# Performance work log

Measured on AMD Instinct MI355X. Metric: run time of the kernel, lower is better.

Reference implementation:

```python
import jax, jax.numpy as jnp
import numpy as np

B, D_MODEL, L = 4, 1024, 2048
D_STATE, D_CONV, EXPAND = 16, 4, 2
D_INNER = EXPAND * D_MODEL
DT_RANK = (D_MODEL + 15) // 16  # 64


def setup_inputs() -> dict:
    key = jax.random.key(0)
    ks = jax.random.split(key, 12)
    s = 0.02
    x = jax.random.normal(ks[0], (B, D_MODEL, L), dtype=jnp.float32)
    in_proj_w = jax.random.normal(ks[1], (2 * D_INNER, D_MODEL), dtype=jnp.float32) * s
    conv_w = jax.random.normal(ks[2], (D_INNER, D_CONV), dtype=jnp.float32) * 0.2
    conv_b = jnp.zeros((D_INNER,), dtype=jnp.float32)
    x_proj_w = jax.random.normal(ks[3], (DT_RANK + 2 * D_STATE, D_INNER), dtype=jnp.float32) * s
    dt_proj_w = jax.random.normal(ks[4], (D_INNER, DT_RANK), dtype=jnp.float32) * (DT_RANK ** -0.5)
    # bias init so softplus(bias) ~ dt in [1e-3, 1e-1], as in mamba_ssm
    dt = jnp.exp(jax.random.uniform(ks[5], (D_INNER,), dtype=jnp.float32)
                 * (np.log(0.1) - np.log(1e-3)) + np.log(1e-3))
    dt_proj_b = dt + jnp.log(-jnp.expm1(-dt))  # inverse softplus
    A_log = jnp.log(jnp.broadcast_to(jnp.arange(1, D_STATE + 1, dtype=jnp.float32),
                                     (D_INNER, D_STATE)))
    D = jnp.ones((D_INNER,), dtype=jnp.float32)
    out_proj_w = jax.random.normal(ks[6], (D_MODEL, D_INNER), dtype=jnp.float32) * s
    proj_w = jax.random.normal(ks[7], (D_MODEL, D_MODEL), dtype=jnp.float32) * s
    proj_b = jnp.zeros((D_MODEL,), dtype=jnp.float32)
    return dict(x=x, in_proj_w=in_proj_w, conv_w=conv_w, conv_b=conv_b,
                x_proj_w=x_proj_w, dt_proj_w=dt_proj_w, dt_proj_b=dt_proj_b,
                A_log=A_log, D=D, out_proj_w=out_proj_w, proj_w=proj_w, proj_b=proj_b)


def _mamba_forward(x, in_proj_w, conv_w, conv_b, x_proj_w, dt_proj_w, dt_proj_b,
                   A_log, D, out_proj_w, proj_w, proj_b):
    xt = jnp.transpose(x, (0, 2, 1))                      # (B, L, d_model)
    xz = jnp.einsum('bld,ed->ble', xt, in_proj_w)         # (B, L, 2*d_inner)
    u, z = jnp.split(xz, 2, axis=-1)                      # each (B, L, d_inner)

    # depthwise causal conv1d along time
    uc = jnp.transpose(u, (0, 2, 1))                      # (B, d_inner, L)
    upad = jnp.pad(uc, ((0, 0), (0, 0), (D_CONV - 1, 0)))
    conv = sum(conv_w[None, :, k, None] * upad[:, :, k:k + L] for k in range(D_CONV))
    conv = conv + conv_b[None, :, None]
    u = jax.nn.silu(jnp.transpose(conv, (0, 2, 1)))       # (B, L, d_inner)

    x_dbl = jnp.einsum('bld,ed->ble', u, x_proj_w)        # (B, L, dt_rank+2n)
    dt_low, Bm, Cm = jnp.split(x_dbl, [DT_RANK, DT_RANK + D_STATE], axis=-1)
    delta = jax.nn.softplus(jnp.einsum('blr,dr->bld', dt_low, dt_proj_w) + dt_proj_b)
    A = -jnp.exp(A_log)                                   # (d_inner, d_state)

    def step(h, inp):
        d_t, B_t, C_t, u_t = inp                          # (B,d),(B,n),(B,n),(B,d)
        dA = jnp.exp(d_t[:, :, None] * A[None])           # (B, d, n)
        dBu = d_t[:, :, None] * B_t[:, None, :] * u_t[:, :, None]
        h = dA * h + dBu
        y_t = jnp.einsum('bdn,bn->bd', h, C_t)
        return h, y_t

    xs = (jnp.transpose(delta, (1, 0, 2)), jnp.transpose(Bm, (1, 0, 2)),
          jnp.transpose(Cm, (1, 0, 2)), jnp.transpose(u, (1, 0, 2)))
    h0 = jnp.zeros((B, D_INNER, D_STATE), dtype=x.dtype)
    _, ys = jax.lax.scan(step, h0, xs)                    # ys: (L, B, d_inner)
    y = jnp.transpose(ys, (1, 0, 2)) + u * D              # (B, L, d_inner)
    y = y * jax.nn.silu(z)

    out = jnp.einsum('bld,ed->ble', y, out_proj_w)        # (B, L, d_model)
    out = jnp.einsum('bld,ed->ble', out, proj_w) + proj_b
    return jnp.transpose(out, (0, 2, 1))                  # (B, d_model, L)


def reference(x, in_proj_w, conv_w, conv_b, x_proj_w, dt_proj_w, dt_proj_b,
              A_log, D, out_proj_w, proj_w, proj_b):
    return _mamba_forward(x, in_proj_w, conv_w, conv_b, x_proj_w, dt_proj_w,
                          dt_proj_b, A_log, D, out_proj_w, proj_w, proj_b)
```

## Files before the change

kernel.cpp:

```cpp
#include <hip/hip_runtime.h>
#include <hip/hip_bf16.h>
#include <math.h>

#define BB 4
#define DMODEL 1024
#define LL 2048
#define DSTATE 16
#define DCONV 4
#define DINNER 2048
#define DTRANK 64
#define BL (BB * LL)
#define NCHUNK 32
#define LCH (LL / NCHUNK)
#define PFPLANE (BB * DINNER * DSTATE)
#define XPN 96
#define XPSPLIT 4
#define XPK (DINNER / XPSPLIT)

typedef unsigned short ushort;
typedef __bf16 bf16x8 __attribute__((ext_vector_type(8)));
typedef float f32x4 __attribute__((ext_vector_type(4)));

__device__ inline ushort f2bf(float f) {
    unsigned int u = __float_as_uint(f);
    u += 0x7fffu + ((u >> 16) & 1u);
    return (ushort)(u >> 16);
}
__device__ inline float bf2f(ushort h) {
    return __uint_as_float(((unsigned int)h) << 16);
}
__device__ inline float softplus_fast(float v) {
    float e = __expf(-fabsf(v));
    return fmaxf(v, 0.f) + __logf(1.f + e);
}

__device__ __forceinline__ void gload16(const ushort* g, ushort* l) {
    __builtin_amdgcn_global_load_lds(
        (__attribute__((address_space(1))) void*)g,
        (__attribute__((address_space(3))) void*)l, 16, 0, 0);
}

__global__ void f32_to_bf16(const float* __restrict__ src, ushort* __restrict__ dst, int n4) {
    int i = blockIdx.x * 256 + threadIdx.x;
    if (i < n4) {
        float4 v = ((const float4*)src)[i];
        ushort4 o;
        o.x = f2bf(v.x); o.y = f2bf(v.y); o.z = f2bf(v.z); o.w = f2bf(v.w);
        ((ushort4*)dst)[i] = o;
    }
}

__global__ void transpose_convert_x(const float* __restrict__ x, ushort* __restrict__ xtb) {
    __shared__ float tile[32][33];
    int b = blockIdx.z;
    int l0 = blockIdx.x * 32;
    int d0 = blockIdx.y * 32;
    int tx = threadIdx.x, ty = threadIdx.y;
    const float* xb = x + (size_t)b * DMODEL * LL;
#pragma unroll
    for (int j = 0; j < 32; j += 8)
        tile[ty + j][tx] = xb[(size_t)(d0 + ty + j) * LL + l0 + tx];
    __syncthreads();
    ushort* xtbb = xtb + (size_t)b * LL * DMODEL;
#pragma unroll
    for (int j = 0; j < 32; j += 8)
        xtbb[(size_t)(l0 + ty + j) * DMODEL + d0 + tx] = f2bf(tile[tx][ty + j]);
}


__global__ __launch_bounds__(256) void gemm_inproj(
    const ushort* __restrict__ A, const ushort* __restrict__ Bw,
    float* __restrict__ U, ushort* __restrict__ Z)
{
    __shared__ __align__(16) ushort As[2][128 * 32];
    __shared__ __align__(16) ushort Bs[2][128 * 32];
    const int tid = threadIdx.x;
    const int m0 = blockIdx.y * 128;
    const int n0 = blockIdx.x * 128;
    const int wave = tid >> 6;
    const int lane = tid & 63;
    const int wm = (wave >> 1) * 64;
    const int wn = (wave & 1) * 64;
    const int fr = lane & 15;
    const int fq = lane >> 4;
    const int fk = fq * 8;
    const int gr = lane >> 2;
    const int gc = (lane & 3) * 8;

    f32x4 acc[4][4];
#pragma unroll
    for (int i = 0; i < 4; ++i)
#pragma unroll
        for (int j = 0; j < 4; ++j)
            acc[i][j] = (f32x4)(0.0f);

    const ushort* Ag0 = A + (size_t)(m0 + wave * 16 + gr) * DMODEL + gc;
    const ushort* Ag1 = Ag0 + (size_t)64 * DMODEL;
    const ushort* Bg0 = Bw + (size_t)(n0 + wave * 16 + gr) * DMODEL + gc;
    const ushort* Bg1 = Bg0 + (size_t)64 * DMODEL;

    auto stage = [&](int s, int k0) {
        gload16(Ag0 + k0, &As[s][wave * 512 + lane * 8]);
        gload16(Ag1 + k0, &As[s][(wave + 4) * 512 + lane * 8]);
        gload16(Bg0 + k0, &Bs[s][wave * 512 + lane * 8]);
        gload16(Bg1 + k0, &Bs[s][(wave + 4) * 512 + lane * 8]);
    };

    stage(0, 0);
    asm volatile("s_waitcnt vmcnt(0)" ::: "memory");
    __builtin_amdgcn_s_barrier();
    asm volatile("" ::: "memory");

    const int NT = DMODEL / 32;
    for (int t = 0; t < NT; ++t) {
        const int cur = t & 1;
        if (t + 1 < NT) stage(cur ^ 1, (t + 1) * 32);
        bf16x8 af[4], bfr[4];
#pragma unroll
        for (int i = 0; i < 4; ++i)
            af[i] = *(const bf16x8*)&As[cur][(wm + i * 16 + fr) * 32 + fk];
#pragma unroll
        for (int j = 0; j < 4; ++j)
            bfr[j] = *(const bf16x8*)&Bs[cur][(wn + j * 16 + fr) * 32 + fk];
#pragma unroll
        for (int i = 0; i < 4; ++i)
#pragma unroll
            for (int j = 0; j < 4; ++j)
                acc[i][j] = __builtin_amdgcn_mfma_f32_16x16x32_bf16(
                    af[i], bfr[j], acc[i][j], 0, 0, 0);
        asm volatile("s_waitcnt vmcnt(0) lgkmcnt(0)" ::: "memory");
        __builtin_amdgcn_s_barrier();
        asm volatile("" ::: "memory");
    }

    if (n0 < DINNER) {
#pragma unroll
        for (int i = 0; i < 4; ++i)
#pragma unroll
            for (int r = 0; r < 4; ++r) {
                int row = m0 + wm + i * 16 + fq * 4 + r;
#pragma unroll
                for (int j = 0; j < 4; ++j)
                    U[(size_t)row * DINNER + n0 + wn + j * 16 + fr] = acc[i][j][r];
            }
    } else {
#pragma unroll
        for (int i = 0; i < 4; ++i)
#pragma unroll
            for (int r = 0; r < 4; ++r) {
                int row = m0 + wm + i * 16 + fq * 4 + r;
#pragma unroll
                for (int j = 0; j < 4; ++j)
                    Z[(size_t)row * DINNER + (n0 - DINNER) + wn + j * 16 + fr] =
                        f2bf(acc[i][j][r]);
            }
    }
}

__global__ __launch_bounds__(256) void gemm_bf16(
    const ushort* __restrict__ A, const ushort* __restrict__ Bw,
    float* __restrict__ C, ushort* __restrict__ Cb,
    const float* __restrict__ bias,
    int M, int N, int K, int lda, int ldb, int ldc, int ldcb, int nbmax, int flags)
{
    __shared__ __align__(16) ushort As[2][128 * 32];
    __shared__ __align__(16) ushort Bs[2][128 * 32];
    const int tid = threadIdx.x;
    const int m0 = blockIdx.y * 128;
    const int n0 = blockIdx.x * 128;
    const int wave = tid >> 6;
    const int lane = tid & 63;
    const int wm = (wave >> 1) * 64;
    const int wn = (wave & 1) * 64;
    const int fr = lane & 15;
    const int fq = lane >> 4;
    const int fk = fq * 8;
    const int gr = lane >> 2;
    const int gc = (lane & 3) * 8;

    f32x4 acc[4][4];
#pragma unroll
    for (int i = 0; i < 4; ++i)
#pragma unroll
        for (int j = 0; j < 4; ++j)
            acc[i][j] = (f32x4)(0.0f);

    const ushort* Ag0 = A + (size_t)(m0 + wave * 16 + gr) * lda + gc;
    const ushort* Ag1 = Ag0 + (size_t)64 * lda;
    const ushort* Bg0 = Bw + (size_t)(n0 + wave * 16 + gr) * ldb + gc;
    const ushort* Bg1 = Bg0 + (size_t)64 * ldb;

    auto stage = [&](int s, int k0) {
        gload16(Ag0 + k0, &As[s][wave * 512 + lane * 8]);
        gload16(Ag1 + k0, &As[s][(wave + 4) * 512 + lane * 8]);
        gload16(Bg0 + k0, &Bs[s][wave * 512 + lane * 8]);
        gload16(Bg1 + k0, &Bs[s][(wave + 4) * 512 + lane * 8]);
    };

    stage(0, 0);
    asm volatile("s_waitcnt vmcnt(0)" ::: "memory");
    __builtin_amdgcn_s_barrier();
    asm volatile("" ::: "memory");

    const int NT = K / 32;
    for (int t = 0; t < NT; ++t) {
        const int cur = t & 1;
        if (t + 1 < NT) stage(cur ^ 1, (t + 1) * 32);
        bf16x8 af[4], bfr[4];
#pragma unroll
        for (int i = 0; i < 4; ++i)
            af[i] = *(const bf16x8*)&As[cur][(wm + i * 16 + fr) * 32 + fk];
#pragma unroll
        for (int j = 0; j < 4; ++j)
            bfr[j] = *(const bf16x8*)&Bs[cur][(wn + j * 16 + fr) * 32 + fk];
#pragma unroll
        for (int i = 0; i < 4; ++i)
#pragma unroll
            for (int j = 0; j < 4; ++j)
                acc[i][j] = __builtin_amdgcn_mfma_f32_16x16x32_bf16(
                    af[i], bfr[j], acc[i][j], 0, 0, 0);
        asm volatile("s_waitcnt vmcnt(0) lgkmcnt(0)" ::: "memory");
        __builtin_amdgcn_s_barrier();
        asm volatile("" ::: "memory");
    }

#pragma unroll
    for (int i = 0; i < 4; ++i) {
#pragma unroll
        for (int r = 0; r < 4; ++r) {
            int row = m0 + wm + i * 16 + fq * 4 + r;
#pragma unroll
            for (int j = 0; j < 4; ++j) {
                int col = n0 + wn + j * 16 + fr;
                if (col < N) {
                    float v = acc[i][j][r];
                    if (flags & 16) {
                        v += bias[row];
                        int bq = col >> 11;
                        int l  = col & (LL - 1);
                        C[(size_t)bq * DMODEL * LL + (size_t)row * LL + l] = v;
                    } else {
                        if (flags & 4) v += bias[col];
                        if (flags & 8) v = softplus_fast(v);
                        if (flags & 1) C[(size_t)row * ldc + col] = v;
                        if ((flags & 2) && col < nbmax)
                            Cb[(size_t)row * ldcb + col] = f2bf(v);
                    }
                }
            }
        }
    }
}

__global__ __launch_bounds__(256) void gemm_xproj(
    const ushort* __restrict__ A, const ushort* __restrict__ Bw,
    float* __restrict__ Pp)
{
    __shared__ __align__(16) ushort As[2][128 * 32];
    __shared__ __align__(16) ushort Bs[2][128 * 32];
    const int tid = threadIdx.x;
    const int kp = blockIdx.x;
    const int m0 = blockIdx.y * 128;
    const int kbase = kp * XPK;
    const int wave = tid >> 6;
    const int lane = tid & 63;
    const int wm = (wave >> 1) * 64;
    const int wn = (wave & 1) * 64;
    const int fr = lane & 15;
    const int fq = lane >> 4;
    const int fk = fq * 8;
    const int gr = lane >> 2;
    const int gc = (lane & 3) * 8;

    f32x4 acc[4][4];
#pragma unroll
    for (int i = 0; i < 4; ++i)
#pragma unroll
        for (int j = 0; j < 4; ++j)
            acc[i][j] = (f32x4)(0.0f);

    const ushort* Ag0 = A + (size_t)(m0 + wave * 16 + gr) * DINNER + kbase + gc;
    const ushort* Ag1 = Ag0 + (size_t)64 * DINNER;
    const ushort* Bg0 = Bw + (size_t)(wave * 16 + gr) * DINNER + kbase + gc;
    const ushort* Bg1 = Bg0 + (size_t)64 * DINNER;

    auto stage = [&](int s, int k0) {
        gload16(Ag0 + k0, &As[s][wave * 512 + lane * 8]);
        gload16(Ag1 + k0, &As[s][(wave + 4) * 512 + lane * 8]);
        gload16(Bg0 + k0, &Bs[s][wave * 512 + lane * 8]);
        gload16(Bg1 + k0, &Bs[s][(wave + 4) * 512 + lane * 8]);
    };

    stage(0, 0);
    asm volatile("s_waitcnt vmcnt(0)" ::: "memory");
    __builtin_amdgcn_s_barrier();
    asm volatile("" ::: "memory");

    const int NT = XPK / 32;
    for (int t = 0; t < NT; ++t) {
        const int cur = t & 1;
        if (t + 1 < NT) stage(cur ^ 1, (t + 1) * 32);
        bf16x8 af[4], bfr[4];
#pragma unroll
        for (int i = 0; i < 4; ++i)
            af[i] = *(const bf16x8*)&As[cur][(wm + i * 16 + fr) * 32 + fk];
#pragma unroll
        for (int j = 0; j < 4; ++j)
            bfr[j] = *(const bf16x8*)&Bs[cur][(wn + j * 16 + fr) * 32 + fk];
#pragma unroll
        for (int i = 0; i < 4; ++i)
#pragma unroll
            for (int j = 0; j < 4; ++j)
                acc[i][j] = __builtin_amdgcn_mfma_f32_16x16x32_bf16(
                    af[i], bfr[j], acc[i][j], 0, 0, 0);
        asm volatile("s_waitcnt vmcnt(0) lgkmcnt(0)" ::: "memory");
        __builtin_amdgcn_s_barrier();
        asm volatile("" ::: "memory");
    }

    float* Cp = Pp + (size_t)kp * ((size_t)BL * XPN);
#pragma unroll
    for (int i = 0; i < 4; ++i) {
#pragma unroll
        for (int r = 0; r < 4; ++r) {
            int row = m0 + wm + i * 16 + fq * 4 + r;
#pragma unroll
            for (int j = 0; j < 4; ++j) {
                int col = wn + j * 16 + fr;
                if (col < XPN)
                    Cp[(size_t)row * XPN + col] = acc[i][j][r];
            }
        }
    }
}

__global__ __launch_bounds__(256) void xproj_reduce(
    const float* __restrict__ Pp, float* __restrict__ xdbl, ushort* __restrict__ dtlow)
{
    int g = blockIdx.x * 256 + threadIdx.x;
    const size_t S = (size_t)BL * XPN;
    float s = (Pp[g] + Pp[g + S]) + (Pp[g + 2 * S] + Pp[g + 3 * S]);
    xdbl[g] = s;
    int row = g / XPN;
    int col = g - row * XPN;
    if (col < DTRANK) dtlow[row * DTRANK + col] = f2bf(s);
}

__global__ void conv_silu(const float* __restrict__ u, const float* __restrict__ cw,
                          const float* __restrict__ cb, ushort* __restrict__ ucb) {
    int idx = blockIdx.x * 256 + threadIdx.x;
    int d4 = idx & (DINNER / 4 - 1);
    int bl = idx >> 9;
    int l = bl & (LL - 1);
    int d = d4 << 2;
    const float* up = u + (size_t)bl * DINNER + d;
    const float4* cwv = (const float4*)cw;
    float4 w0 = cwv[d], w1 = cwv[d + 1], w2 = cwv[d + 2], w3 = cwv[d + 3];
    float4 bv = *(const float4*)(cb + d);
    float4 t = *(const float4*)(up);
    float4 a;
    a.x = fmaf(w0.w, t.x, bv.x);
    a.y = fmaf(w1.w, t.y, bv.y);
    a.z = fmaf(w2.w, t.z, bv.z);
    a.w = fmaf(w3.w, t.w, bv.w);
    if (l >= 1) {
        t = *(const float4*)(up - DINNER);
        a.x = fmaf(w0.z, t.x, a.x); a.y = fmaf(w1.z, t.y, a.y);
        a.z = fmaf(w2.z, t.z, a.z); a.w = fmaf(w3.z, t.w, a.w);
    }
    if (l >= 2) {
        t = *(const float4*)(up - 2 * DINNER);
        a.x = fmaf(w0.y, t.x, a.x); a.y = fmaf(w1.y, t.y, a.y);
        a.z = fmaf(w2.y, t.z, a.z); a.w = fmaf(w3.y, t.w, a.w);
    }
    if (l >= 3) {
        t = *(const float4*)(up - 3 * DINNER);
        a.x = fmaf(w0.x, t.x, a.x); a.y = fmaf(w1.x, t.y, a.y);
        a.z = fmaf(w2.x, t.z, a.z); a.w = fmaf(w3.x, t.w, a.w);
    }
    ushort4 o;
    o.x = f2bf(a.x / (1.f + __expf(-a.x)));
    o.y = f2bf(a.y / (1.f + __expf(-a.y)));
    o.z = f2bf(a.z / (1.f + __expf(-a.z)));
    o.w = f2bf(a.w / (1.f + __expf(-a.w)));
    ((ushort4*)ucb)[idx] = o;
}

__global__ __launch_bounds__(256) void scan_phase1(
    const ushort* __restrict__ delta16, const float* __restrict__ xdbl,
    const ushort* __restrict__ ucb, const float* __restrict__ A_log,
    float* __restrict__ P, float* __restrict__ F)
{
    int g = blockIdx.x * 256 + threadIdx.x;
    int d = g & (DINNER - 1);
    int c = (g >> 11) & (NCHUNK - 1);
    int b = g >> 16;

    float An[16], p[16], f[16];
    const float4* alp = (const float4*)(A_log + (size_t)d * DSTATE);
#pragma unroll
    for (int q = 0; q < 4; ++q) {
        float4 a = alp[q];
        An[q * 4 + 0] = -__expf(a.x); An[q * 4 + 1] = -__expf(a.y);
        An[q * 4 + 2] = -__expf(a.z); An[q * 4 + 3] = -__expf(a.w);
    }
#pragma unroll
    for (int n = 0; n < 16; ++n) { p[n] = 1.f; f[n] = 0.f; }

    size_t bl0 = (size_t)b * LL + (size_t)c * LCH;
    const ushort* dptr = delta16 + bl0 * DINNER + d;
    const ushort* uptr = ucb + bl0 * DINNER + d;
    const float* xptr = xdbl + bl0 * 96 + DTRANK;

#pragma unroll 2
    for (int l = 0; l < LCH; ++l) {
        float dv = bf2f(dptr[(size_t)l * DINNER]);
        float du = dv * bf2f(uptr[(size_t)l * DINNER]);
        float4 B0 = *(const float4*)(xptr + (size_t)l * 96);
        float4 B1 = *(const float4*)(xptr + (size_t)l * 96 + 4);
        float4 B2 = *(const float4*)(xptr + (size_t)l * 96 + 8);
        float4 B3 = *(const float4*)(xptr + (size_t)l * 96 + 12);
        float Bv[16] = {B0.x, B0.y, B0.z, B0.w, B1.x, B1.y, B1.z, B1.w,
                        B2.x, B2.y, B2.z, B2.w, B3.x, B3.y, B3.z, B3.w};
#pragma unroll
        for (int n = 0; n < 16; ++n) {
            float dA = __expf(dv * An[n]);
            f[n] = fmaf(dA, f[n], du * Bv[n]);
            p[n] *= dA;
        }
    }
    size_t o = (size_t)c * PFPLANE + ((size_t)(b * DINNER + d) << 4);
#pragma unroll
    for (int q = 0; q < 4; ++q) {
        *(float4*)(P + o + q * 4) = make_float4(p[q*4], p[q*4+1], p[q*4+2], p[q*4+3]);
        *(float4*)(F + o + q * 4) = make_float4(f[q*4], f[q*4+1], f[q*4+2], f[q*4+3]);
    }
}

__global__ __launch_bounds__(256) void scan_phase2(
    float* __restrict__ P, const float* __restrict__ F)
{
    int g = blockIdx.x * 256 + threadIdx.x;
    float h = 0.f;
#pragma unroll
    for (int c = 0; c < NCHUNK; ++c) {
        size_t idx = (size_t)c * PFPLANE + g;
        float pv = P[idx];
        float fv = F[idx];
        P[idx] = h;
        h = fmaf(pv, h, fv);
    }
}

__global__ __launch_bounds__(256) void scan_phase3(
    const ushort* __restrict__ delta16, const float* __restrict__ xdbl,
    const ushort* __restrict__ ucb, const ushort* __restrict__ zb,
    const float* __restrict__ A_log, const float* __restrict__ Dp,
    const float* __restrict__ Hin, ushort* __restrict__ ybf)
{
    int g = blockIdx.x * 256 + threadIdx.x;
    int d = g & (DINNER - 1);
    int c = (g >> 11) & (NCHUNK - 1);
    int b = g >> 16;

    float An[16], h[16];
    const float4* alp = (const float4*)(A_log + (size_t)d * DSTATE);
#pragma unroll
    for (int q = 0; q < 4; ++q) {
        float4 a = alp[q];
        An[q * 4 + 0] = -__expf(a.x); An[q * 4 + 1] = -__expf(a.y);
        An[q * 4 + 2] = -__expf(a.z); An[q * 4 + 3] = -__expf(a.w);
    }
    size_t o = (size_t)c * PFPLANE + ((size_t)(b * DINNER + d) << 4);
#pragma unroll
    for (int q = 0; q < 4; ++q) {
        float4 hv = *(const float4*)(Hin + o + q * 4);
        h[q * 4 + 0] = hv.x; h[q * 4 + 1] = hv.y;
        h[q * 4 + 2] = hv.z; h[q * 4 + 3] = hv.w;
    }
    float Dd = Dp[d];

    size_t bl0 = (size_t)b * LL + (size_t)c * LCH;
    const ushort* dptr = delta16 + bl0 * DINNER + d;
    const ushort* uptr = ucb + bl0 * DINNER + d;
    const ushort* zptr = zb + bl0 * DINNER + d;
    const float* xptr = xdbl + bl0 * 96 + DTRANK;
    ushort* yptr = ybf + bl0 * DINNER + d;

#pragma unroll 2
    for (int l = 0; l < LCH; ++l) {
        float dv = bf2f(dptr[(size_t)l * DINNER]);
        float uv = bf2f(uptr[(size_t)l * DINNER]);
        float zv = bf2f(zptr[(size_t)l * DINNER]);
        float du = dv * uv;
        float4 B0 = *(const float4*)(xptr + (size_t)l * 96);
        float4 B1 = *(const float4*)(xptr + (size_t)l * 96 + 4);
        float4 B2 = *(const float4*)(xptr + (size_t)l * 96 + 8);
        float4 B3 = *(const float4*)(xptr + (size_t)l * 96 + 12);
        float4 C0 = *(const float4*)(xptr + (size_t)l * 96 + 16);
        float4 C1 = *(const float4*)(xptr + (size_t)l * 96 + 20);
        float4 C2 = *(const float4*)(xptr + (size_t)l * 96 + 24);
        float4 C3 = *(const float4*)(xptr + (size_t)l * 96 + 28);
        float Bv[16] = {B0.x, B0.y, B0.z, B0.w, B1.x, B1.y, B1.z, B1.w,
                        B2.x, B2.y, B2.z, B2.w, B3.x, B3.y, B3.z, B3.w};
        float Cv[16] = {C0.x, C0.y, C0.z, C0.w, C1.x, C1.y, C1.z, C1.w,
                        C2.x, C2.y, C2.z, C2.w, C3.x, C3.y, C3.z, C3.w};
        float y0 = 0.f, y1 = 0.f, y2 = 0.f, y3 = 0.f;
#pragma unroll
        for (int n = 0; n < 4; ++n) {
            float dA0 = __expf(dv * An[n]);
            float dA1 = __expf(dv * An[n + 4]);
            float dA2 = __expf(dv * An[n + 8]);
            float dA3 = __expf(dv * An[n + 12]);
            h[n]      = fmaf(dA0, h[n],      du * Bv[n]);
            h[n + 4]  = fmaf(dA1, h[n + 4],  du * Bv[n + 4]);
            h[n + 8]  = fmaf(dA2, h[n + 8],  du * Bv[n + 8]);
            h[n + 12] = fmaf(dA3, h[n + 12], du * Bv[n + 12]);
            y0 = fmaf(h[n],      Cv[n],      y0);
            y1 = fmaf(h[n + 4],  Cv[n + 4],  y1);
            y2 = fmaf(h[n + 8],  Cv[n + 8],  y2);
            y3 = fmaf(h[n + 12], Cv[n + 12], y3);
        }
        float y = (y0 + y1) + (y2 + y3);
        float sz = zv / (1.f + __expf(-zv));
        yptr[(size_t)l * DINNER] = f2bf((y + uv * Dd) * sz);
    }
}

extern "C" void kernel_launch(void* const* d_in, const int* in_sizes, int n_in,
                              void* d_out, int out_size, void* d_ws, size_t ws_size,
                              hipStream_t stream) {
    const float* x         = (const float*)d_in[0];
    const float* in_proj_w = (const float*)d_in[1];
    const float* conv_w    = (const float*)d_in[2];
    const float* conv_b    = (const float*)d_in[3];
    const float* x_proj_w  = (const float*)d_in[4];
    const float* dt_proj_w = (const float*)d_in[5];
    const float* dt_proj_b = (const float*)d_in[6];
    const float* A_log     = (const float*)d_in[7];
    const float* Dp        = (const float*)d_in[8];
    const float* out_proj_w= (const float*)d_in[9];
    const float* proj_w    = (const float*)d_in[10];
    const float* proj_b    = (const float*)d_in[11];
    float* out = (float*)d_out;

    char* wsb = (char*)d_ws;
    float*  bufU    = (float*)(wsb);
    ushort* delta16 = (ushort*)(wsb);
    float*  Pbuf    = (float*)(wsb + ((size_t)32 << 20));
    float*  xprojP  = (float*)(wsb + ((size_t)32 << 20));
    float*  Fbuf    = (float*)(wsb + ((size_t)48 << 20));
    ushort* zb      = (ushort*)(wsb + ((size_t)64 << 20));
    ushort* xtb     = (ushort*)(wsb + ((size_t)96 << 20));
    ushort* ucb     = (ushort*)(wsb + ((size_t)96 << 20));
    ushort* ybf     = (ushort*)(wsb + ((size_t)128 << 20));
    float*  xdbl    = (float*)(wsb + ((size_t)160 << 20));
    ushort* dtlow   = (ushort*)(wsb + ((size_t)163 << 20));
    ushort* wip     = (ushort*)(wsb + ((size_t)164 << 20));
    ushort* wxp     = wip + (size_t)4194304;
    ushort* wdt     = wxp + (size_t)196608;
    ushort* wop     = wdt + (size_t)131072;
    ushort* wpj     = wop + (size_t)2097152;
    ushort* out1b   = (ushort*)(wsb + ((size_t)32 << 20));

    f32_to_bf16<<<dim3(4096), 256, 0, stream>>>(in_proj_w, wip, 1048576);
    f32_to_bf16<<<dim3(192),  256, 0, stream>>>(x_proj_w,  wxp, 49152);
    f32_to_bf16<<<dim3(128),  256, 0, stream>>>(dt_proj_w, wdt, 32768);
    f32_to_bf16<<<dim3(2048), 256, 0, stream>>>(out_proj_w, wop, 524288);
    f32_to_bf16<<<dim3(1024), 256, 0, stream>>>(proj_w,    wpj, 262144);

    transpose_convert_x<<<dim3(LL / 32, DMODEL / 32, BB), dim3(32, 8), 0, stream>>>(x, xtb);

    gemm_inproj<<<dim3(2 * DINNER / 128, BL / 128), 256, 0, stream>>>(
        xtb, wip, bufU, zb);

    conv_silu<<<dim3(BL * DINNER / 4 / 256), 256, 0, stream>>>(bufU, conv_w, conv_b, ucb);

    gemm_xproj<<<dim3(XPSPLIT, BL / 128), 256, 0, stream>>>(ucb, wxp, xprojP);
    xproj_reduce<<<dim3(BL * XPN / 256), 256, 0, stream>>>(xprojP, xdbl, dtlow);

    gemm_bf16<<<dim3(DINNER / 128, BL / 128), 256, 0, stream>>>(
        dtlow, wdt, nullptr, delta16, dt_proj_b,
        BL, DINNER, DTRANK, DTRANK, DTRANK, 0, DINNER, DINNER, 2 | 4 | 8);

    const int scan_threads = BB * NCHUNK * DINNER;
    scan_phase1<<<dim3(scan_threads / 256), 256, 0, stream>>>(
        delta16, xdbl, ucb, A_log, Pbuf, Fbuf);
    scan_phase2<<<dim3(PFPLANE / 256), 256, 0, stream>>>(Pbuf, Fbuf);
    scan_phase3<<<dim3(scan_threads / 256), 256, 0, stream>>>(
        delta16, xdbl, ucb, zb, A_log, Dp, Pbuf, ybf);

    gemm_bf16<<<dim3(DMODEL / 128, BL / 128), 256, 0, stream>>>(
        ybf, wop, nullptr, out1b, nullptr,
        BL, DMODEL, DINNER, DINNER, DINNER, 0, DMODEL, DMODEL, 2);

    gemm_bf16<<<dim3(BL / 128, DMODEL / 128), 256, 0, stream>>>(
        wpj, out1b, out, nullptr, proj_b,
        DMODEL, BL, DMODEL, DMODEL, DMODEL, 0, 0, 0, 16);
}
```

Baseline: 620.2 us.

## Fold out_proj and proj weights into one GEMM and enlarge in_proj tiles

Result: no change. 610.9 us (-1.5%).

```diff
diff --git a/kernel.cpp b/kernel.cpp
--- a/kernel.cpp
+++ b/kernel.cpp
@@ -67,43 +67,57 @@
         xtbb[(size_t)(l0 + ty + j) * DMODEL + d0 + tx] = f2bf(tile[tx][ty + j]);
 }
 
-
-__global__ __launch_bounds__(256) void gemm_inproj(
+__global__ void transpose_convert_w(const float* __restrict__ in, ushort* __restrict__ outb,
+                                    int R, int C) {
+    __shared__ float tile[32][33];
+    int c0 = blockIdx.x * 32;
+    int r0 = blockIdx.y * 32;
+    int tx = threadIdx.x, ty = threadIdx.y;
+#pragma unroll
+    for (int j = 0; j < 32; j += 8)
+        tile[ty + j][tx] = in[(size_t)(r0 + ty + j) * C + c0 + tx];
+    __syncthreads();
+#pragma unroll
+    for (int j = 0; j < 32; j += 8)
+        outb[(size_t)(c0 + ty + j) * R + r0 + tx] = f2bf(tile[tx][ty + j]);
+}
+
+__global__ __launch_bounds__(512) void gemm_inproj256(
     const ushort* __restrict__ A, const ushort* __restrict__ Bw,
     float* __restrict__ U, ushort* __restrict__ Z)
 {
-    __shared__ __align__(16) ushort As[2][128 * 32];
-    __shared__ __align__(16) ushort Bs[2][128 * 32];
+    __shared__ __align__(16) ushort As[2][256 * 32];
+    __shared__ __align__(16) ushort Bs[2][256 * 32];
     const int tid = threadIdx.x;
-    const int m0 = blockIdx.y * 128;
-    const int n0 = blockIdx.x * 128;
+    const int m0 = blockIdx.y * 256;
+    const int n0 = blockIdx.x * 256;
     const int wave = tid >> 6;
     const int lane = tid & 63;
-    const int wm = (wave >> 1) * 64;
-    const int wn = (wave & 1) * 64;
+    const int wm = (wave >> 2) * 128;
+    const int wn = (wave & 3) * 64;
     const int fr = lane & 15;
     const int fq = lane >> 4;
     const int fk = fq * 8;
     const int gr = lane >> 2;
     const int gc = (lane & 3) * 8;
 
-    f32x4 acc[4][4];
-#pragma unroll
-    for (int i = 0; i < 4; ++i)
+    f32x4 acc[8][4];
+#pragma unroll
+    for (int i = 0; i < 8; ++i)
 #pragma unroll
         for (int j = 0; j < 4; ++j)
             acc[i][j] = (f32x4)(0.0f);
 
     const ushort* Ag0 = A + (size_t)(m0 + wave * 16 + gr) * DMODEL + gc;
-    const ushort* Ag1 = Ag0 + (size_t)64 * DMODEL;
+    const ushort* Ag1 = Ag0 + (size_t)128 * DMODEL;
     const ushort* Bg0 = Bw + (size_t)(n0 + wave * 16 + gr) * DMODEL + gc;
-    const ushort* Bg1 = Bg0 + (size_t)64 * DMODEL;
+    const ushort* Bg1 = Bg0 + (size_t)128 * DMODEL;
 
     auto stage = [&](int s, int k0) {
         gload16(Ag0 + k0, &As[s][wave * 512 + lane * 8]);
-        gload16(Ag1 + k0, &As[s][(wave + 4) * 512 + lane * 8]);
+        gload16(Ag1 + k0, &As[s][4096 + wave * 512 + lane * 8]);
         gload16(Bg0 + k0, &Bs[s][wave * 512 + lane * 8]);
-        gload16(Bg1 + k0, &Bs[s][(wave + 4) * 512 + lane * 8]);
+        gload16(Bg1 + k0, &Bs[s][4096 + wave * 512 + lane * 8]);
     };
 
     stage(0, 0);
@@ -115,15 +129,15 @@
     for (int t = 0; t < NT; ++t) {
         const int cur = t & 1;
         if (t + 1 < NT) stage(cur ^ 1, (t + 1) * 32);
-        bf16x8 af[4], bfr[4];
-#pragma unroll
-        for (int i = 0; i < 4; ++i)
+        bf16x8 af[8], bfr[4];
+#pragma unroll
+        for (int i = 0; i < 8; ++i)
             af[i] = *(const bf16x8*)&As[cur][(wm + i * 16 + fr) * 32 + fk];
 #pragma unroll
         for (int j = 0; j < 4; ++j)
             bfr[j] = *(const bf16x8*)&Bs[cur][(wn + j * 16 + fr) * 32 + fk];
 #pragma unroll
-        for (int i = 0; i < 4; ++i)
+        for (int i = 0; i < 8; ++i)
 #pragma unroll
             for (int j = 0; j < 4; ++j)
                 acc[i][j] = __builtin_amdgcn_mfma_f32_16x16x32_bf16(
@@ -135,7 +149,7 @@
 
     if (n0 < DINNER) {
 #pragma unroll
-        for (int i = 0; i < 4; ++i)
+        for (int i = 0; i < 8; ++i)
 #pragma unroll
             for (int r = 0; r < 4; ++r) {
                 int row = m0 + wm + i * 16 + fq * 4 + r;
@@ -145,7 +159,7 @@
             }
     } else {
 #pragma unroll
-        for (int i = 0; i < 4; ++i)
+        for (int i = 0; i < 8; ++i)
 #pragma unroll
             for (int r = 0; r < 4; ++r) {
                 int row = m0 + wm + i * 16 + fq * 4 + r;
@@ -557,22 +571,27 @@
     float*  xdbl    = (float*)(wsb + ((size_t)160 << 20));
     ushort* dtlow   = (ushort*)(wsb + ((size_t)163 << 20));
     ushort* wip     = (ushort*)(wsb + ((size_t)164 << 20));
+    ushort* W2      = wip;
     ushort* wxp     = wip + (size_t)4194304;
     ushort* wdt     = wxp + (size_t)196608;
-    ushort* wop     = wdt + (size_t)131072;
-    ushort* wpj     = wop + (size_t)2097152;
-    ushort* out1b   = (ushort*)(wsb + ((size_t)32 << 20));
+    ushort* wopT    = wdt + (size_t)131072;
+    ushort* wpj     = wopT + (size_t)2097152;
 
     f32_to_bf16<<<dim3(4096), 256, 0, stream>>>(in_proj_w, wip, 1048576);
     f32_to_bf16<<<dim3(192),  256, 0, stream>>>(x_proj_w,  wxp, 49152);
     f32_to_bf16<<<dim3(128),  256, 0, stream>>>(dt_proj_w, wdt, 32768);
-    f32_to_bf16<<<dim3(2048), 256, 0, stream>>>(out_proj_w, wop, 524288);
+    transpose_convert_w<<<dim3(DINNER / 32, DMODEL / 32), dim3(32, 8), 0, stream>>>(
+        out_proj_w, wopT, DMODEL, DINNER);
     f32_to_bf16<<<dim3(1024), 256, 0, stream>>>(proj_w,    wpj, 262144);
 
     transpose_convert_x<<<dim3(LL / 32, DMODEL / 32, BB), dim3(32, 8), 0, stream>>>(x, xtb);
 
-    gemm_inproj<<<dim3(2 * DINNER / 128, BL / 128), 256, 0, stream>>>(
+    gemm_inproj256<<<dim3(2 * DINNER / 256, BL / 256), 512, 0, stream>>>(
         xtb, wip, bufU, zb);
+
+    gemm_bf16<<<dim3(DINNER / 128, DMODEL / 128), 256, 0, stream>>>(
+        wpj, wopT, nullptr, W2, nullptr,
+        DMODEL, DINNER, DMODEL, DMODEL, DMODEL, 0, DINNER, DINNER, 2);
 
     conv_silu<<<dim3(BL * DINNER / 4 / 256), 256, 0, stream>>>(bufU, conv_w, conv_b, ucb);
 
@@ -590,11 +609,7 @@
     scan_phase3<<<dim3(scan_threads / 256), 256, 0, stream>>>(
         delta16, xdbl, ucb, zb, A_log, Dp, Pbuf, ybf);
 
-    gemm_bf16<<<dim3(DMODEL / 128, BL / 128), 256, 0, stream>>>(
-        ybf, wop, nullptr, out1b, nullptr,
-        BL, DMODEL, DINNER, DINNER, DINNER, 0, DMODEL, DMODEL, 2);
-
     gemm_bf16<<<dim3(BL / 128, DMODEL / 128), 256, 0, stream>>>(
-        wpj, out1b, out, nullptr, proj_b,
-        DMODEL, BL, DMODEL, DMODEL, DMODEL, 0, 0, 0, 16);
-}
+        W2, ybf, out, nullptr, proj_b,
+        DMODEL, BL, DINNER, DINNER, DINNER, 0, 0, 0, 16);
+}
```
